# Kernel optimization log

Hardware: AMD Instinct MI355X
Metric: run time of the kernel (lower is better)

## Reference

```python
import jax, jax.numpy as jnp
import numpy as np

N_NODES = 50000
N_EDGES = 1_600_000
IN_FEAT = 128
OUT_FEAT = 128
NUM_RELS = 8


def setup_inputs() -> dict:
    key = jax.random.key(0)
    k_h, k_src, k_dst, k_et, k_nrm, k_w, k_b = jax.random.split(key, 7)
    h = jax.random.normal(k_h, (N_NODES, IN_FEAT), dtype=jnp.float32)
    src = jax.random.randint(k_src, (N_EDGES,), 0, N_NODES, dtype=jnp.int32)
    dst = jax.random.randint(k_dst, (N_EDGES,), 0, N_NODES, dtype=jnp.int32)
    etype = jax.random.randint(k_et, (N_EDGES,), 0, NUM_RELS, dtype=jnp.int32)
    norm = jax.random.uniform(k_nrm, (N_EDGES, 1), dtype=jnp.float32)
    W = jax.random.normal(k_w, (NUM_RELS, IN_FEAT, OUT_FEAT), dtype=jnp.float32)
    b = jax.random.normal(k_b, (NUM_RELS, OUT_FEAT), dtype=jnp.float32)
    return {"h": h, "src": src, "dst": dst, "etype": etype, "norm": norm, "W": W, "b": b}


def reference(h, src, dst, etype, norm, W, b):
    # Per-relation node transforms: [R, N, out]. Same math as the DGL code
    # (which computes src_h @ W for all relations then gathers the right one
    # per edge), but computed once per node instead of once per edge.
    H = jnp.einsum('ni,rio->rno', h, W)
    # Gather per-edge transformed message, add per-relation bias, scale by norm.
    msg = (H[etype, src] + b[etype]) * norm  # [E, out]
    # Sum-reduce messages into destination nodes.
    out = jax.ops.segment_sum(msg, dst, num_segments=h.shape[0])  # [N, out]
    return jax.nn.relu(out)
```

## Files before the change

kernel.cpp:

```cpp
#include <hip/hip_runtime.h>

#define N_NODES_C   50000
#define N_EDGES_C   1600000
#define FEAT        128
#define NREL        8
#define NBUCKETS    400000
#define KTOT        1024
#define TILE        16

#define WS_COUNTS   0
#define WS_OFFSETS  400000
#define WS_RANK     2000016
#define WS_BSUM     3600016
#define WS_BOFF     3602064
#define WS_SORTED   3604112
#define WS_HB       10004112
#define WS_WT       22804112
#define WS_NEEDED   23066256

typedef __attribute__((ext_vector_type(8))) short bf16x8;
typedef __attribute__((ext_vector_type(4))) float f32x4;

__device__ __forceinline__ unsigned short f2bf(float f) {
    unsigned u = __float_as_uint(f);
    return (unsigned short)((u + 0x7fffu + ((u >> 16) & 1u)) >> 16);
}
__device__ __forceinline__ float bf2f(unsigned short b) {
    return __uint_as_float((unsigned)b << 16);
}
__device__ __forceinline__ float lo16(unsigned u) { return __uint_as_float(u << 16); }
__device__ __forceinline__ float hi16(unsigned u) { return __uint_as_float(u & 0xffff0000u); }

__global__ void k_prep(const float* __restrict__ h, const float* __restrict__ W,
                       unsigned* __restrict__ counts, unsigned short* __restrict__ hb,
                       unsigned short* __restrict__ wt) {
    int b = blockIdx.x, t = threadIdx.x;
    if (b < 3125) {
        int i = (b * 256 + t) * 8;
        float4 v0 = *(const float4*)&h[i];
        float4 v1 = *(const float4*)&h[i + 4];
        uint4 o;
        o.x = (unsigned)f2bf(v0.x) | ((unsigned)f2bf(v0.y) << 16);
        o.y = (unsigned)f2bf(v0.z) | ((unsigned)f2bf(v0.w) << 16);
        o.z = (unsigned)f2bf(v1.x) | ((unsigned)f2bf(v1.y) << 16);
        o.w = (unsigned)f2bf(v1.z) | ((unsigned)f2bf(v1.w) << 16);
        *(uint4*)&hb[i] = o;
    } else if (b < 3125 + 98) {
        int i = (b - 3125) * 256 + t;
        if (i < 25000) ((uint4*)counts)[i] = make_uint4(0u, 0u, 0u, 0u);
    } else {
        int i = (b - 3223) * 256 + t;
        int n = i >> 10, rk = i & 1023;
        wt[i] = f2bf(W[rk * FEAT + n]);
    }
}

__global__ void k_hist(const int* __restrict__ dst, const int* __restrict__ et,
                       unsigned* __restrict__ counts, unsigned char* __restrict__ rank) {
    int e = blockIdx.x * 256 + threadIdx.x;
    if (e < N_EDGES_C) {
        int key = dst[e] * NREL + et[e];
        int sh = 8 * (key & 3);
        unsigned old = atomicAdd(&counts[key >> 2], 1u << sh);
        rank[e] = (unsigned char)((old >> sh) & 0xffu);
    }
}

__global__ void k_scan_a(const unsigned* __restrict__ counts, unsigned* __restrict__ bsum) {
    __shared__ unsigned s[1024];
    int t = threadIdx.x;
    int i = blockIdx.x * 1024 + t;
    unsigned v = 0;
    if (i < NBUCKETS) v = (counts[i >> 2] >> (8 * (i & 3))) & 0xffu;
    s[t] = v;
    __syncthreads();
    for (int o = 512; o > 0; o >>= 1) {
        if (t < o) s[t] += s[t + o];
        __syncthreads();
    }
    if (t == 0) bsum[blockIdx.x] = s[0];
}

__global__ void k_scan_b(const unsigned* __restrict__ bsum, unsigned* __restrict__ boff, int nb) {
    __shared__ unsigned s[512];
    int t = threadIdx.x;
    unsigned v = (t < nb) ? bsum[t] : 0u;
    s[t] = v;
    __syncthreads();
    for (int o = 1; o < 512; o <<= 1) {
        unsigned u = (t >= o) ? s[t - o] : 0u;
        __syncthreads();
        s[t] += u;
        __syncthreads();
    }
    if (t < nb) boff[t] = s[t] - v;
}

__global__ void k_scan_c(const unsigned* __restrict__ counts, const unsigned* __restrict__ boff,
                         unsigned* __restrict__ offsets) {
    __shared__ unsigned s[1024];
    int t = threadIdx.x;
    int i = blockIdx.x * 1024 + t;
    unsigned v = 0;
    if (i < NBUCKETS) v = (counts[i >> 2] >> (8 * (i & 3))) & 0xffu;
    s[t] = v;
    __syncthreads();
    for (int o = 1; o < 1024; o <<= 1) {
        unsigned u = (t >= o) ? s[t - o] : 0u;
        __syncthreads();
        s[t] += u;
        __syncthreads();
    }
    if (i < NBUCKETS) offsets[i] = boff[blockIdx.x] + s[t] - v;
    if (i == NBUCKETS) offsets[i] = N_EDGES_C;
}

__global__ void k_scatter(const int* __restrict__ src, const int* __restrict__ dst,
                          const int* __restrict__ et, const float* __restrict__ norm,
                          const unsigned* __restrict__ offsets,
                          const unsigned char* __restrict__ rank,
                          unsigned* __restrict__ sorted) {
    int e = blockIdx.x * 256 + threadIdx.x;
    if (e < N_EDGES_C) {
        int key = dst[e] * NREL + et[e];
        unsigned pos = offsets[key] + (unsigned)rank[e];
        sorted[pos] = ((unsigned)src[e] << 16) | (unsigned)f2bf(norm[e]);
    }
}

__global__ __launch_bounds__(512) void k_fused(const unsigned* __restrict__ sorted,
                                               const unsigned* __restrict__ offsets,
                                               const unsigned short* __restrict__ hb,
                                               const unsigned short* __restrict__ wt,
                                               const float* __restrict__ bias,
                                               float* __restrict__ out) {
    __shared__ char At[32768];
    __shared__ float csLds[TILE][NREL];
    int t = threadIdx.x, w = t >> 6, lane = t & 63;
    int node0 = blockIdx.x * TILE;
    int grp = lane >> 4, ln16 = lane & 15;

    int kbase = (node0 + 2 * w) * NREL;
    unsigned bnds = offsets[kbase + (lane <= 16 ? lane : 16)];
    unsigned pp   = __shfl(bnds, 0);
    unsigned send = __shfl(bnds, 16);
    int j = 0;
    unsigned bend = __shfl(bnds, 1);
    float a0 = 0.f, a1 = 0.f, cs = 0.f;

#define FLUSHJ(JJ, A0, A1, CS)                                                 \
    do {                                                                       \
        int row_ = 2 * w + ((JJ) >> 3);                                        \
        int jr_  = (JJ) & 7;                                                   \
        *(unsigned*)(At + row_ * 2048 +                                        \
                     ((jr_ * 256 + lane * 4) ^ ((row_ & 7) << 4))) =           \
            (unsigned)f2bf(A0) | ((unsigned)f2bf(A1) << 16);                   \
        if (lane == 0) csLds[row_][jr_] = (CS);                                \
    } while (0)

    unsigned rec[8];
#pragma unroll
    for (int u = 0; u < 8; u++) {
        unsigned q = pp + u;
        rec[u] = sorted[q < N_EDGES_C ? q : (N_EDGES_C - 1)];
    }

    while (pp < send) {
        unsigned hv[8];
#pragma unroll
        for (int u = 0; u < 8; u++)
            hv[u] = *(const unsigned*)&hb[(size_t)(rec[u] >> 16) * FEAT + lane * 2];
        unsigned nrec[8];
#pragma unroll
        for (int u = 0; u < 8; u++) {
            unsigned q = pp + 8 + u;
            nrec[u] = sorted[q < N_EDGES_C ? q : (N_EDGES_C - 1)];
        }
#pragma unroll
        for (int u = 0; u < 8; u++) {
            if (pp >= send) break;
            while (pp >= bend) {
                FLUSHJ(j, a0, a1, cs);
                a0 = a1 = cs = 0.f;
                j++;
                bend = __shfl(bnds, j + 1 <= 16 ? j + 1 : 16);
            }
            float nv = bf2f((unsigned short)(rec[u] & 0xffffu));
            a0 += nv * lo16(hv[u]);
            a1 += nv * hi16(hv[u]);
            cs += nv;
            pp++;
        }
#pragma unroll
        for (int u = 0; u < 8; u++) rec[u] = nrec[u];
    }
    while (j < 16) {
        FLUSHJ(j, a0, a1, cs);
        a0 = a1 = cs = 0.f;
        j++;
    }
#undef FLUSHJ
    __syncthreads();

    f32x4 acc = (f32x4){0.f, 0.f, 0.f, 0.f};
    const unsigned short* wcol = wt + (size_t)(w * 16 + ln16) * KTOT + grp * 8;
#pragma unroll 8
    for (int ks = 0; ks < 32; ks++) {
        bf16x8 af = *(const bf16x8*)(At + ln16 * 2048 +
                                     ((ks * 64 + grp * 16) ^ ((ln16 & 7) << 4)));
        bf16x8 bf = *(const bf16x8*)(wcol + ks * 32);
        acc = __builtin_amdgcn_mfma_f32_16x16x32_bf16(af, bf, acc, 0, 0, 0);
    }

#pragma unroll
    for (int i = 0; i < 4; i++) {
        int rl = grp * 4 + i;
        int g  = node0 + rl;
        int col = w * 16 + ln16;
        float v = acc[i];
#pragma unroll
        for (int rr = 0; rr < NREL; rr++) v += csLds[rl][rr] * bias[rr * FEAT + col];
        out[(size_t)g * FEAT + col] = fmaxf(v, 0.f);
    }
}

extern "C" void kernel_launch(void* const* d_in, const int* in_sizes, int n_in,
                              void* d_out, int out_size, void* d_ws, size_t ws_size,
                              hipStream_t stream) {
    const float* h    = (const float*)d_in[0];
    const int*   src  = (const int*)d_in[1];
    const int*   dst  = (const int*)d_in[2];
    const int*   et   = (const int*)d_in[3];
    const float* norm = (const float*)d_in[4];
    const float* W    = (const float*)d_in[5];
    const float* b    = (const float*)d_in[6];
    float*       out  = (float*)d_out;

    if (ws_size < (size_t)WS_NEEDED) return;

    char* ws = (char*)d_ws;
    unsigned*       counts  = (unsigned*)(ws + WS_COUNTS);
    unsigned*       offsets = (unsigned*)(ws + WS_OFFSETS);
    unsigned char*  rank    = (unsigned char*)(ws + WS_RANK);
    unsigned*       bsum    = (unsigned*)(ws + WS_BSUM);
    unsigned*       boff    = (unsigned*)(ws + WS_BOFF);
    unsigned*       sorted  = (unsigned*)(ws + WS_SORTED);
    unsigned short* hb      = (unsigned short*)(ws + WS_HB);
    unsigned short* wt      = (unsigned short*)(ws + WS_WT);

    int nb = (NBUCKETS + 1023) / 1024;

    k_prep<<<3125 + 98 + 512, 256, 0, stream>>>(h, W, counts, hb, wt);
    k_hist<<<6250, 256, 0, stream>>>(dst, et, counts, rank);
    k_scan_a<<<nb, 1024, 0, stream>>>(counts, bsum);
    k_scan_b<<<1, 512, 0, stream>>>(bsum, boff, nb);
    k_scan_c<<<nb, 1024, 0, stream>>>(counts, boff, offsets);
    k_scatter<<<6250, 256, 0, stream>>>(src, dst, et, norm, offsets, rank, sorted);

    k_fused<<<N_NODES_C / TILE, 512, 0, stream>>>(sorted, offsets, hb, wt, b, out);
}
```

Measured before the change: 265.4 us.

## Load edge records wave-wide and broadcast via readlane; merge histogram with prep

The fused gather loop now loads 64 sorted edge records with one coalesced per-lane load and broadcasts each to the wave with readlane. This replaces the earlier scheme in which every lane loaded the same 8 records redundantly. The next 64-record chunk is prefetched while the current one is consumed. Separately, the counts zeroing moves to its own small kernel, and the histogram pass is merged with the h/W bf16 conversion into one launch. This saves a launch and lets the atomic histogram overlap with the conversion work, at the cost of one extra tiny kernel and a goto-based early exit.

```diff
diff --git a/kernel.cpp b/kernel.cpp
--- a/kernel.cpp
+++ b/kernel.cpp
@@ -31,12 +31,26 @@
 __device__ __forceinline__ float lo16(unsigned u) { return __uint_as_float(u << 16); }
 __device__ __forceinline__ float hi16(unsigned u) { return __uint_as_float(u & 0xffff0000u); }
 
-__global__ void k_prep(const float* __restrict__ h, const float* __restrict__ W,
-                       unsigned* __restrict__ counts, unsigned short* __restrict__ hb,
-                       unsigned short* __restrict__ wt) {
+__global__ void k_zero(unsigned* __restrict__ counts) {
+    int i = blockIdx.x * 256 + threadIdx.x;
+    if (i < 25000) ((uint4*)counts)[i] = make_uint4(0u, 0u, 0u, 0u);
+}
+
+__global__ void k_histprep(const int* __restrict__ dst, const int* __restrict__ et,
+                           unsigned* __restrict__ counts, unsigned char* __restrict__ rank,
+                           const float* __restrict__ h, unsigned short* __restrict__ hb,
+                           const float* __restrict__ W, unsigned short* __restrict__ wt) {
     int b = blockIdx.x, t = threadIdx.x;
-    if (b < 3125) {
-        int i = (b * 256 + t) * 8;
+    if (b < 6250) {
+        int e = b * 256 + t;
+        if (e < N_EDGES_C) {
+            int key = dst[e] * NREL + et[e];
+            int sh = 8 * (key & 3);
+            unsigned old = atomicAdd(&counts[key >> 2], 1u << sh);
+            rank[e] = (unsigned char)((old >> sh) & 0xffu);
+        }
+    } else if (b < 6250 + 3125) {
+        int i = ((b - 6250) * 256 + t) * 8;
         float4 v0 = *(const float4*)&h[i];
         float4 v1 = *(const float4*)&h[i + 4];
         uint4 o;
@@ -45,24 +59,10 @@
         o.z = (unsigned)f2bf(v1.x) | ((unsigned)f2bf(v1.y) << 16);
         o.w = (unsigned)f2bf(v1.z) | ((unsigned)f2bf(v1.w) << 16);
         *(uint4*)&hb[i] = o;
-    } else if (b < 3125 + 98) {
-        int i = (b - 3125) * 256 + t;
-        if (i < 25000) ((uint4*)counts)[i] = make_uint4(0u, 0u, 0u, 0u);
     } else {
-        int i = (b - 3223) * 256 + t;
+        int i = (b - 9375) * 256 + t;
         int n = i >> 10, rk = i & 1023;
         wt[i] = f2bf(W[rk * FEAT + n]);
-    }
-}
-
-__global__ void k_hist(const int* __restrict__ dst, const int* __restrict__ et,
-                       unsigned* __restrict__ counts, unsigned char* __restrict__ rank) {
-    int e = blockIdx.x * 256 + threadIdx.x;
-    if (e < N_EDGES_C) {
-        int key = dst[e] * NREL + et[e];
-        int sh = 8 * (key & 3);
-        unsigned old = atomicAdd(&counts[key >> 2], 1u << sh);
-        rank[e] = (unsigned char)((old >> sh) & 0xffu);
     }
 }
 
@@ -145,7 +145,7 @@
     unsigned pp   = __shfl(bnds, 0);
     unsigned send = __shfl(bnds, 16);
     int j = 0;
-    unsigned bend = __shfl(bnds, 1);
+    unsigned bend = (unsigned)__builtin_amdgcn_readlane((int)bnds, 1);
     float a0 = 0.f, a1 = 0.f, cs = 0.f;
 
 #define FLUSHJ(JJ, A0, A1, CS)                                                 \
@@ -158,41 +158,44 @@
         if (lane == 0) csLds[row_][jr_] = (CS);                                \
     } while (0)
 
-    unsigned rec[8];
-#pragma unroll
-    for (int u = 0; u < 8; u++) {
-        unsigned q = pp + u;
-        rec[u] = sorted[q < N_EDGES_C ? q : (N_EDGES_C - 1)];
-    }
-
-    while (pp < send) {
-        unsigned hv[8];
-#pragma unroll
-        for (int u = 0; u < 8; u++)
-            hv[u] = *(const unsigned*)&hb[(size_t)(rec[u] >> 16) * FEAT + lane * 2];
-        unsigned nrec[8];
-#pragma unroll
-        for (int u = 0; u < 8; u++) {
-            unsigned q = pp + 8 + u;
-            nrec[u] = sorted[q < N_EDGES_C ? q : (N_EDGES_C - 1)];
+    {
+        unsigned q0 = pp + lane;
+        unsigned recv = sorted[q0 < N_EDGES_C ? q0 : (N_EDGES_C - 1)];
+        unsigned wstart = pp;
+        while (wstart < send) {
+            unsigned qn = wstart + 64 + lane;
+            unsigned recv_n = sorted[qn < N_EDGES_C ? qn : (N_EDGES_C - 1)];
+#pragma unroll 1
+            for (int b = 0; b < 8; b++) {
+                unsigned hv[8];
+                float nvv[8];
+#pragma unroll
+                for (int u = 0; u < 8; u++) {
+                    unsigned ru = (unsigned)__builtin_amdgcn_readlane((int)recv, b * 8 + u);
+                    nvv[u] = __uint_as_float((ru & 0xffffu) << 16);
+                    const unsigned short* rp = hb + (size_t)(ru >> 16) * FEAT;
+                    hv[u] = *(const unsigned*)(rp + lane * 2);
+                }
+#pragma unroll
+                for (int u = 0; u < 8; u++) {
+                    unsigned gpos = wstart + (unsigned)(b * 8 + u);
+                    if (gpos >= send) goto stream_done;
+                    while (gpos >= bend) {
+                        FLUSHJ(j, a0, a1, cs);
+                        a0 = a1 = cs = 0.f;
+                        j++;
+                        bend = (unsigned)__builtin_amdgcn_readlane(
+                            (int)bnds, j < 16 ? j + 1 : 16);
+                    }
+                    a0 += nvv[u] * lo16(hv[u]);
+                    a1 += nvv[u] * hi16(hv[u]);
+                    cs += nvv[u];
+                }
+            }
+            wstart += 64;
+            recv = recv_n;
         }
-#pragma unroll
-        for (int u = 0; u < 8; u++) {
-            if (pp >= send) break;
-            while (pp >= bend) {
-                FLUSHJ(j, a0, a1, cs);
-                a0 = a1 = cs = 0.f;
-                j++;
-                bend = __shfl(bnds, j + 1 <= 16 ? j + 1 : 16);
-            }
-            float nv = bf2f((unsigned short)(rec[u] & 0xffffu));
-            a0 += nv * lo16(hv[u]);
-            a1 += nv * hi16(hv[u]);
-            cs += nv;
-            pp++;
-        }
-#pragma unroll
-        for (int u = 0; u < 8; u++) rec[u] = nrec[u];
+    stream_done:;
     }
     while (j < 16) {
         FLUSHJ(j, a0, a1, cs);
@@ -250,8 +253,9 @@
 
     int nb = (NBUCKETS + 1023) / 1024;
 
-    k_prep<<<3125 + 98 + 512, 256, 0, stream>>>(h, W, counts, hb, wt);
-    k_hist<<<6250, 256, 0, stream>>>(dst, et, counts, rank);
+    k_zero<<<98, 256, 0, stream>>>(counts);
+    k_histprep<<<6250 + 3125 + 512, 256, 0, stream>>>(dst, et, counts, rank,
+                                                      h, hb, W, wt);
     k_scan_a<<<nb, 1024, 0, stream>>>(counts, bsum);
     k_scan_b<<<1, 512, 0, stream>>>(bsum, boff, nb);
     k_scan_c<<<nb, 1024, 0, stream>>>(counts, boff, offsets);
```

After: 262.6 us. Within noise of the previous version (-1.0%).
